# Performance work log

Measured on AMD Instinct MI355X. Metric: run time of the kernel, lower is better.

Reference implementation:

```python
import jax, jax.numpy as jnp
import numpy as np

EPS = 1e-5
HEADS, DK, DV = 8, 32, 32


def conv3x3(x, w, b):
    # regular (non-depthwise, despite the name) 3x3 conv, stride 1, padding 1
    y = jax.lax.conv_general_dilated(
        x, w, window_strides=(1, 1), padding='SAME',
        dimension_numbers=('NCHW', 'OIHW', 'NCHW'))
    return y + b[None, :, None, None]


def setup_inputs() -> dict:
    key = jax.random.key(0)
    ks = jax.random.split(key, 16)
    C = 256
    d = {}
    d['x'] = jax.random.normal(ks[0], (8, C, 32, 32), jnp.float32)
    s_lin = 1.0 / np.sqrt(C)
    s_conv = 1.0 / np.sqrt(C * 9)
    d['Wq'] = jax.random.normal(ks[1], (C, HEADS * DK), jnp.float32) * s_lin
    d['bq'] = jnp.zeros((HEADS * DK,), jnp.float32)
    d['conv_k_w'] = jax.random.normal(ks[2], (C, C, 3, 3), jnp.float32) * s_conv
    d['conv_k_b'] = jnp.zeros((C,), jnp.float32)
    d['Wk'] = jax.random.normal(ks[3], (C, HEADS * DK), jnp.float32) * s_lin
    d['bk'] = jnp.zeros((HEADS * DK,), jnp.float32)
    d['conv_v_w'] = jax.random.normal(ks[4], (C, C, 3, 3), jnp.float32) * s_conv
    d['conv_v_b'] = jnp.zeros((C,), jnp.float32)
    d['Wv'] = jax.random.normal(ks[5], (C, HEADS * DV), jnp.float32) * s_lin
    d['bv'] = jnp.zeros((HEADS * DV,), jnp.float32)
    d['Wo'] = jax.random.normal(ks[6], (HEADS * DV, C), jnp.float32) * s_lin
    d['bo'] = jnp.zeros((C,), jnp.float32)
    d['B'] = jax.random.normal(ks[7], (1, HEADS, 1024, 1024), jnp.float32) * 0.02
    return d


def reference(x, Wq, bq, conv_k_w, conv_k_b, Wk, bk, conv_v_w, conv_v_b, Wv, bv, Wo, bo, B):
    b, c, h, w = x.shape
    hw = h * w
    xr = x.reshape(b, c, hw).transpose(0, 2, 1)  # [b, hw, c]
    # F.layer_norm with normalized_shape == full shape: whole-tensor stats, no affine
    m = jnp.mean(xr)
    v = jnp.mean((xr - m) ** 2)
    xn = (xr - m) * jax.lax.rsqrt(v + EPS)

    q = (xn @ Wq + bq).reshape(b, hw, HEADS, DK).transpose(0, 2, 1, 3)  # [b,H,hw,dk]

    k = conv3x3(x, conv_k_w, conv_k_b)  # stride 1 -> same spatial size (per source)
    k = k.reshape(b, c, hw).transpose(0, 2, 1)
    k = (k @ Wk + bk).reshape(b, hw, HEADS, DK).transpose(0, 2, 1, 3)

    vv = conv3x3(x, conv_v_w, conv_v_b)
    vv = vv.reshape(b, c, hw).transpose(0, 2, 1)
    vv = (vv @ Wv + bv).reshape(b, hw, HEADS, DV).transpose(0, 2, 1, 3)

    scale = DK ** (-0.5)
    attn = jnp.einsum('bhid,bhjd->bhij', q, k) * scale + B  # [b,H,hw,hw]
    attn = jax.nn.softmax(attn, axis=-1)
    out = jnp.einsum('bhij,bhjd->bhid', attn, vv)  # [b,H,hw,dv]
    out = out.transpose(0, 2, 1, 3).reshape(b, hw, HEADS * DV)
    out = out @ Wo + bo  # [b, hw, c]
    # faithful to torch .view(b, c, h, w): raw reshape, NO transpose
    out = out.reshape(b, c, h, w)
    return out + x
```

## Files before the change

### kernel.cpp

```cpp
#include <hip/hip_runtime.h>
#include <hip/hip_bf16.h>
#include <math.h>

#define B_     8
#define C_     256
#define HW_    1024
#define NTOT   (B_*C_*HW_)
#define HEADS_ 8
#define DK_    32
#define SCALE_ 0.17677669529663687f

#define F_STATS 0
#define F_PART  16
#define F_YK2   8192
#define F_YV2   (F_YK2 + NTOT)
#define F_XB    (F_YV2 + NTOT)
#define F_WT    (F_XB + NTOT/2)
#define F_QB    (F_WT + 589824)
#define F_KB    (F_QB + NTOT/2)
#define F_VT    (F_KB + NTOT/2)

typedef float f32x4 __attribute__((ext_vector_type(4)));
typedef short short8 __attribute__((ext_vector_type(8)));

__device__ __forceinline__ short bf16s(float f) {
    __hip_bfloat16 h = __float2bfloat16(f);
    return *(short*)&h;
}
__device__ __forceinline__ unsigned pack_bf16(float a, float b) {
    unsigned ua = (unsigned short)bf16s(a);
    unsigned ub = (unsigned short)bf16s(b);
    return ua | (ub << 16);
}
__device__ __forceinline__ void gload_lds16(const short* g, short* l) {
    __builtin_amdgcn_global_load_lds(
        (const __attribute__((address_space(1))) unsigned*)g,
        (__attribute__((address_space(3))) unsigned*)l, 16, 0, 0);
}

__global__ void k_prep_x(const float* __restrict__ x, short* __restrict__ xb,
                         float* __restrict__ part) {
    __shared__ short t[32 * 258];
    __shared__ float ls[4], ls2[4];
    int b = blockIdx.x >> 5, p0 = (blockIdx.x & 31) << 5;
    int tid = threadIdx.x;
    float s = 0.f, s2 = 0.f;
    for (int i = tid; i < 256 * 32; i += 256) {
        int ci = i >> 5, p = i & 31;
        float v = x[(b * C_ + ci) * HW_ + p0 + p];
        s += v; s2 += v * v;
        t[p * 258 + ci] = bf16s(v);
    }
    for (int o = 32; o; o >>= 1) { s += __shfl_down(s, o); s2 += __shfl_down(s2, o); }
    int wid = tid >> 6, lane = tid & 63;
    if (lane == 0) { ls[wid] = s; ls2[wid] = s2; }
    __syncthreads();
    if (tid == 0) {
        float a = 0.f, bb = 0.f;
        for (int i = 0; i < 4; i++) { a += ls[i]; bb += ls2[i]; }
        part[blockIdx.x * 2] = a; part[blockIdx.x * 2 + 1] = bb;
    }
    for (int i = tid; i < 32 * 256; i += 256) {
        int p = i >> 8, ci = i & 255;
        xb[(b * HW_ + p0 + p) * C_ + ci] = t[p * 258 + ci];
    }
}

__global__ void k_stats(const float* __restrict__ part, float* __restrict__ stats) {
    __shared__ float ls[256], ls2[256];
    float s = part[2 * threadIdx.x], s2 = part[2 * threadIdx.x + 1];
    ls[threadIdx.x] = s; ls2[threadIdx.x] = s2;
    __syncthreads();
    for (int off = 128; off; off >>= 1) {
        if (threadIdx.x < off) { ls[threadIdx.x] += ls[threadIdx.x + off]; ls2[threadIdx.x] += ls2[threadIdx.x + off]; }
        __syncthreads();
    }
    if (threadIdx.x == 0) {
        float m = ls[0] / (float)NTOT;
        float var = ls2[0] / (float)NTOT - m * m;
        stats[0] = m;
        stats[1] = rsqrtf(var + 1e-5f);
    }
}

__global__ void k_prep_w(const float* __restrict__ wk, const float* __restrict__ wv,
                         short* __restrict__ wt) {
    int idx = blockIdx.x * 256 + threadIdx.x;
    int ci0 = (idx << 2) & 255;
    int rest = idx >> 6;
    int n = rest & 511, tap = rest >> 9;
    const float* src = (n < 256) ? (wk + (n * C_) * 9) : (wv + ((n - 256) * C_) * 9);
    short4 o;
    short* op = (short*)&o;
    for (int u = 0; u < 4; u++)
        op[u] = bf16s(src[(ci0 + u) * 9 + tap]);
    *(short4*)&wt[((tap * 512 + n) * C_) + ci0] = o;
}

__global__ void k_prep_pw(const float* __restrict__ Wq, const float* __restrict__ Wk,
                          const float* __restrict__ Wv, const float* __restrict__ Wo,
                          short* __restrict__ wt4) {
    __shared__ short t[64 * 66];
    int mi = blockIdx.x >> 4, tl = blockIdx.x & 15;
    int c0 = (tl >> 2) * 64, e0 = (tl & 3) * 64;
    const float* W = mi == 0 ? Wq : mi == 1 ? Wk : mi == 2 ? Wv : Wo;
    int tid = threadIdx.x;
    for (int i = tid; i < 4096; i += 256) {
        int cl = i >> 6, el = i & 63;
        t[cl * 66 + el] = bf16s(W[(c0 + cl) * 256 + e0 + el]);
    }
    __syncthreads();
    for (int i = tid; i < 4096; i += 256) {
        int el = i >> 6, cl = i & 63;
        wt4[mi * 65536 + (e0 + el) * 256 + c0 + cl] = t[cl * 66 + el];
    }
}

__global__ void k_prep_beta(const float* __restrict__ Wq, const float* __restrict__ bq,
                            const float* __restrict__ stats, float* __restrict__ beta0) {
    __shared__ float ps[1024];
    int t = threadIdx.x, e = t & 255, part = t >> 8;
    float s = 0.f;
    for (int c = part * 64; c < part * 64 + 64; c++) s += Wq[c * 256 + e];
    ps[t] = s;
    __syncthreads();
    if (t < 256) {
        float cs = ps[t] + ps[t + 256] + ps[t + 512] + ps[t + 768];
        beta0[t] = (bq[t] - stats[0] * stats[1] * cs) * SCALE_;
    }
}

__device__ __forceinline__ int a_off(int slot, int chunk) {
    int c = chunk ^ (slot & 3);
    int s = slot ^ ((slot >> 2) & 1);
    return s * 64 + c * 16;
}

__global__ __launch_bounds__(512, 4)
void k_conv_mfma(const short* __restrict__ xb, const short* __restrict__ wt,
                 const float* __restrict__ bk, const float* __restrict__ bv,
                 short* __restrict__ yk2b, short* __restrict__ yv2b) {
    __shared__ short a_sh[204 * 32];
    __shared__ short b_sh[9 * 2048];
    int bid = blockIdx.x;
    int nt = bid & 7, pt = (bid >> 3) & 7, b = bid >> 6;
    int R0 = pt * 4;
    int tid = threadIdx.x;
    int w = tid >> 6, l = tid & 63;
    int wm = w >> 1, wn = w & 1;
    int col16 = l & 15, kq = l >> 4;

    int offs[2], loffs[2];
    #pragma unroll
    for (int it = 0; it < 2; it++) {
        int i = tid + it * 512;
        if (i < 816) {
            int slot = i >> 2, chunk = i & 3;
            int ty = slot / 34, tx = slot - ty * 34;
            int Y = R0 - 1 + ty, X = tx - 1;
            offs[it] = ((unsigned)Y < 32u && (unsigned)X < 32u)
                       ? ((b * HW_ + Y * 32 + X) * C_ + chunk * 8) : -1;
            loffs[it] = a_off(slot, chunk);
        } else { offs[it] = -1; loffs[it] = -1; }
    }

    int bgoff[5];
    int nbj = 0;
    #pragma unroll 1
    for (int j = w; j < 36; j += 8) {
        int S = j * 64 + l;
        int tap = S >> 8, s = S & 255;
        int colb = s >> 2, kqs = s & 3;
        int kq2 = kqs ^ ((colb >> 1) & 3);
        bgoff[nbj++] = (tap * 512 + nt * 64 + colb) * C_ + kq2 * 8;
    }

    f32x4 acc[2][2];
    #pragma unroll
    for (int m = 0; m < 2; m++)
        #pragma unroll
        for (int n = 0; n < 2; n++) acc[m][n] = (f32x4)0.f;

    int sr[2];
    #pragma unroll
    for (int nf = 0; nf < 2; nf++) {
        int colb = wn * 32 + nf * 16 + col16;
        sr[nf] = (colb << 2) | (kq ^ ((colb >> 1) & 3));
    }

    {
        short8 sv[2];
        #pragma unroll
        for (int it = 0; it < 2; it++)
            sv[it] = (offs[it] >= 0) ? *(const short8*)(xb + offs[it]) : (short8)0;
        int jj = 0;
        #pragma unroll 1
        for (int j = w; j < 36; j += 8, jj++)
            gload_lds16(wt + bgoff[jj], b_sh + j * 512);
        #pragma unroll
        for (int it = 0; it < 2; it++)
            if (loffs[it] >= 0) *(short8*)((char*)a_sh + loffs[it]) = sv[it];
    }
    __syncthreads();

    #pragma unroll 1
    for (int step = 0; step < 8; step++) {
        const char* ab = (const char*)a_sh;
        const char* bbp = (const char*)b_sh;
        #pragma unroll
        for (int tap = 0; tap < 9; tap++) {
            const int dyi = tap / 3, dxi = tap % 3;
            short8 af[2], bf[2];
            #pragma unroll
            for (int mf = 0; mf < 2; mf++) {
                int slot = (wm + dyi) * 34 + mf * 16 + col16 + dxi;
                af[mf] = *(const short8*)(ab + a_off(slot, kq));
            }
            #pragma unroll
            for (int nf = 0; nf < 2; nf++)
                bf[nf] = *(const short8*)(bbp + tap * 4096 + sr[nf] * 16);
            #pragma unroll
            for (int mf = 0; mf < 2; mf++)
                #pragma unroll
                for (int nf = 0; nf < 2; nf++)
                    acc[mf][nf] = __builtin_amdgcn_mfma_f32_16x16x32_bf16(af[mf], bf[nf], acc[mf][nf], 0, 0, 0);
        }
        if (step < 7) {
            int ci0n = step * 32 + 32;
            __syncthreads();
            short8 sv[2];
            #pragma unroll
            for (int it = 0; it < 2; it++)
                sv[it] = (offs[it] >= 0) ? *(const short8*)(xb + offs[it] + ci0n) : (short8)0;
            int jj = 0;
            #pragma unroll 1
            for (int j = w; j < 36; j += 8, jj++)
                gload_lds16(wt + bgoff[jj] + ci0n, b_sh + j * 512);
            #pragma unroll
            for (int it = 0; it < 2; it++)
                if (loffs[it] >= 0) *(short8*)((char*)a_sh + loffs[it]) = sv[it];
            __syncthreads();
        }
    }

    const bool isv = (nt >= 4);
    short* dst = isv ? yv2b : yk2b;
    const float* bias = isv ? bv : bk;
    int cbase = (nt & 3) * 64 + wn * 32 + col16;
    #pragma unroll
    for (int nf = 0; nf < 2; nf++) {
        int co = cbase + nf * 16;
        float bi = bias[co];
        #pragma unroll
        for (int mf = 0; mf < 2; mf++) {
            #pragma unroll
            for (int r = 0; r < 4; r++) {
                int pixel = pt * 128 + wm * 32 + mf * 16 + kq * 4 + r;
                dst[(b * HW_ + pixel) * C_ + co] = bf16s(acc[mf][nf][r] + bi);
            }
        }
    }
}

__global__ void k_proj_mfma(const short* __restrict__ xb,
                            const short* __restrict__ yk2b, const short* __restrict__ yv2b,
                            const short* __restrict__ wt4,
                            const float* __restrict__ bkp, const float* __restrict__ bvp,
                            const float* __restrict__ stats, const float* __restrict__ beta0,
                            short* __restrict__ qb, short* __restrict__ kb,
                            short* __restrict__ vt) {
    __shared__ char smem[17408];
    int pj = blockIdx.x, pt = blockIdx.y, b = blockIdx.z;
    int p0 = pt * 32;
    int tid = threadIdx.x, w = tid >> 6, l = tid & 63;
    int c16 = l & 15, kq = l >> 4;

    const short* src = pj == 0 ? xb : (pj == 1 ? yk2b : yv2b);
    #pragma unroll
    for (int it = 0; it < 4; it++) {
        int i = it * 256 + tid;
        int slab = i >> 7, rem = i & 127, slot = rem >> 2, chunk = rem & 3;
        short8 v = *(const short8*)(src + ((b * HW_ + p0 + slot) * C_ + slab * 32 + chunk * 8));
        *(short8*)(smem + slab * 2048 + a_off(slot, chunk)) = v;
    }
    __syncthreads();

    const short* wt_p = wt4 + pj * 65536;
    f32x4 acc[2][4];
    #pragma unroll
    for (int m = 0; m < 2; m++)
        #pragma unroll
        for (int n = 0; n < 4; n++) acc[m][n] = (f32x4)0.f;

    for (int s = 0; s < 8; s++) {
        short8 af[2], bf[4];
        #pragma unroll
        for (int mf = 0; mf < 2; mf++)
            af[mf] = *(const short8*)(smem + s * 2048 + a_off(mf * 16 + c16, kq));
        #pragma unroll
        for (int nf = 0; nf < 4; nf++)
            bf[nf] = *(const short8*)(wt_p + (w * 64 + nf * 16 + c16) * 256 + s * 32 + kq * 8);
        #pragma unroll
        for (int mf = 0; mf < 2; mf++)
            #pragma unroll
            for (int nf = 0; nf < 4; nf++)
                acc[mf][nf] = __builtin_amdgcn_mfma_f32_16x16x32_bf16(af[mf], bf[nf], acc[mf][nf], 0, 0, 0);
    }

    float alpha = (pj == 0) ? stats[1] * SCALE_ : 1.f;
    float beta[4];
    #pragma unroll
    for (int nf = 0; nf < 4; nf++) {
        int e = w * 64 + nf * 16 + c16;
        beta[nf] = (pj == 0) ? beta0[e] : (pj == 1 ? bkp[e] : bvp[e]);
    }
    __syncthreads();

    short* rp = (short*)smem + w * 2176;
    if (pj < 2) {
        #pragma unroll
        for (int mf = 0; mf < 2; mf++)
            #pragma unroll
            for (int nf = 0; nf < 4; nf++)
                #pragma unroll
                for (int rg = 0; rg < 4; rg++) {
                    int px = mf * 16 + kq * 4 + rg, el = nf * 16 + c16;
                    rp[px * 66 + el] = bf16s(alpha * acc[mf][nf][rg] + beta[nf]);
                }
        __syncthreads();
        short* dst = (pj == 0) ? qb : kb;
        #pragma unroll
        for (int j = 0; j < 4; j++) {
            int px = j * 8 + (l >> 3), el = (l & 7) * 8;
            short8 v = *(const short8*)(rp + px * 66 + el);
            int e = w * 64 + el, h = e >> 5, d = e & 31;
            *(short8*)(dst + ((b * 8 + h) * HW_ + p0 + px) * DK_ + d) = v;
        }
    } else {
        #pragma unroll
        for (int mf = 0; mf < 2; mf++)
            #pragma unroll
            for (int nf = 0; nf < 4; nf++)
                #pragma unroll
                for (int rg = 0; rg < 4; rg++) {
                    int px = mf * 16 + kq * 4 + rg, el = nf * 16 + c16;
                    rp[el * 34 + px] = bf16s(acc[mf][nf][rg] + beta[nf]);
                }
        __syncthreads();
        #pragma unroll
        for (int j = 0; j < 4; j++) {
            int el = j * 16 + (l >> 2), px = (l & 3) * 8;
            short8 v = *(const short8*)(rp + el * 34 + px);
            int e = w * 64 + el, h = e >> 5, d = e & 31;
            *(short8*)(vt + ((b * 8 + h) * DK_ + d) * HW_ + p0 + px) = v;
        }
    }
}

__global__ __launch_bounds__(256, 4)
void k_attn(const short* __restrict__ qb, const short* __restrict__ kb,
            const short* __restrict__ vt, const float* __restrict__ Bb,
            short* __restrict__ ao) {
    __shared__ __align__(16) short Ks[128 * 32];
    __shared__ __align__(16) short Vs[32 * 128];
    int bid = blockIdx.x;
    int h = bid & 7, b = (bid >> 3) & 7, qt = bid >> 6;
    int bh = b * HEADS_ + h;
    int tid = threadIdx.x, w = tid >> 6, l = tid & 63;
    int g = l >> 4, c16 = l & 15;

    int qrow = qt * 64 + w * 16 + c16;
    short8 qf = *(const short8*)(qb + (bh * HW_ + qrow) * DK_ + g * 8);
    const float* Brow = Bb + (h * HW_ + qrow) * HW_;

    float4 breg[8];
    #pragma unroll
    for (int mt = 0; mt < 8; mt++)
        breg[mt] = *(const float4*)(Brow + mt * 16 + g * 4);

    float m_run = -1e30f, l_run = 0.f;
    f32x4 ot[2];
    ot[0] = (f32x4)0.f; ot[1] = (f32x4)0.f;

    int vrow = tid >> 4, vch = tid & 15;
    int vrow2 = (tid + 256) >> 4, vch2 = (tid + 256) & 15;
    const short* kbase = kb + bh * HW_ * DK_;

    for (int kv0 = 0; kv0 < HW_; kv0 += 128) {
        __syncthreads();
        gload_lds16(kbase + kv0 * DK_ + (w * 2) * 512 + l * 8, Ks + (w * 2) * 512);
        gload_lds16(kbase + kv0 * DK_ + (w * 2 + 1) * 512 + l * 8, Ks + (w * 2 + 1) * 512);
        {
            short8 v0 = *(const short8*)(vt + (bh * DK_ + vrow) * HW_ + kv0 + vch * 8);
            short8 v1 = *(const short8*)(vt + (bh * DK_ + vrow2) * HW_ + kv0 + vch2 * 8);
            *(short8*)((char*)Vs + vrow * 256 + ((vch * 16) ^ ((vrow & 7) << 4))) = v0;
            *(short8*)((char*)Vs + vrow2 * 256 + ((vch2 * 16) ^ ((vrow2 & 7) << 4))) = v1;
        }
        __syncthreads();

        f32x4 st[8];
        __builtin_amdgcn_s_setprio(1);
        #pragma unroll
        for (int mt = 0; mt < 8; mt++) {
            f32x4 acc;
            acc[0] = breg[mt].x; acc[1] = breg[mt].y; acc[2] = breg[mt].z; acc[3] = breg[mt].w;
            short8 kf = *(const short8*)(Ks + (mt * 16 + c16) * DK_ + g * 8);
            st[mt] = __builtin_amdgcn_mfma_f32_16x16x32_bf16(kf, qf, acc, 0, 0, 0);
        }
        __builtin_amdgcn_s_setprio(0);
        if (kv0 + 128 < HW_) {
            #pragma unroll
            for (int mt = 0; mt < 8; mt++)
                breg[mt] = *(const float4*)(Brow + kv0 + 128 + mt * 16 + g * 4);
        }

        float pmax = st[0][0];
        #pragma unroll
        for (int mt = 0; mt < 8; mt++)
            #pragma unroll
            for (int rg = 0; rg < 4; rg++) pmax = fmaxf(pmax, st[mt][rg]);
        pmax = fmaxf(pmax, __shfl_xor(pmax, 16));
        pmax = fmaxf(pmax, __shfl_xor(pmax, 32));
        if (!__all(pmax <= m_run + 8.f)) {
            float mnew = fmaxf(m_run, pmax);
            float f = __expf(m_run - mnew);
            m_run = mnew;
            l_run *= f;
            int fv = __float_as_int(f);
            #pragma unroll
            for (int rg = 0; rg < 4; rg++) {
                float fr = __int_as_float(__builtin_amdgcn_ds_bpermute((g * 4 + rg) << 2, fv));
                ot[0][rg] *= fr;
                ot[1][rg] *= fr;
            }
        }
        float s = 0.f;
        #pragma unroll
        for (int mt = 0; mt < 8; mt++)
            #pragma unroll
            for (int rg = 0; rg < 4; rg++) {
                float e_ = __expf(st[mt][rg] - m_run);
                st[mt][rg] = e_;
                s += e_;
            }
        s += __shfl_xor(s, 16);
        s += __shfl_xor(s, 32);
        l_run += s;

        short8 pa[4];
        #pragma unroll
        for (int kt = 0; kt < 4; kt++) {
            unsigned u0 = pack_bf16(st[2 * kt][0], st[2 * kt][1]);
            unsigned u1 = pack_bf16(st[2 * kt][2], st[2 * kt][3]);
            unsigned u2 = pack_bf16(st[2 * kt + 1][0], st[2 * kt + 1][1]);
            unsigned u3 = pack_bf16(st[2 * kt + 1][2], st[2 * kt + 1][3]);
            unsigned* pu = (unsigned*)&pa[kt];
            pu[0] = u0; pu[1] = u1; pu[2] = u2; pu[3] = u3;
        }

        __builtin_amdgcn_s_setprio(1);
        #pragma unroll
        for (int kt = 0; kt < 4; kt++) {
            #pragma unroll
            for (int nt = 0; nt < 2; nt++) {
                int dv = c16 + 16 * nt;
                int X0 = kt * 64 + 8 * g;
                int X1 = X0 + 32;
                int a0 = dv * 256 + ((((X0 >> 4) ^ (dv & 7)) << 4) | (X0 & 15));
                int a1 = dv * 256 + ((((X1 >> 4) ^ (dv & 7)) << 4) | (X1 & 15));
                unsigned long long lo = *(const unsigned long long*)((char*)Vs + a0);
                unsigned long long hi = *(const unsigned long long*)((char*)Vs + a1);
                short8 vf;
                *(unsigned long long*)&vf = lo;
                *((unsigned long long*)&vf + 1) = hi;
                ot[nt] = __builtin_amdgcn_mfma_f32_16x16x32_bf16(pa[kt], vf, ot[nt], 0, 0, 0);
            }
        }
        __builtin_amdgcn_s_setprio(0);
    }

    float linv = 1.f / l_run;
    int lrv = __float_as_int(linv);
    #pragma unroll
    for (int rg = 0; rg < 4; rg++) {
        float li = __int_as_float(__builtin_amdgcn_ds_bpermute((g * 4 + rg) << 2, lrv));
        int qg = qt * 64 + w * 16 + g * 4 + rg;
        #pragma unroll
        for (int nt = 0; nt < 2; nt++)
            ao[(b * HW_ + qg) * C_ + h * DK_ + nt * 16 + c16] = bf16s(ot[nt][rg] * li);
    }
}

__global__ void k_out_mfma(const short* __restrict__ aob, const short* __restrict__ wot,
                           const float* __restrict__ bo, const float* __restrict__ x,
                           float* __restrict__ out) {
    __shared__ char smem[16384];
    int pt = blockIdx.x, b = blockIdx.y;
    int p0 = pt * 32;
    int tid = threadIdx.x, w = tid >> 6, l = tid & 63;
    int c16 = l & 15, kq = l >> 4;

    #pragma unroll
    for (int it = 0; it < 4; it++) {
        int i = it * 256 + tid;
        int slab = i >> 7, rem = i & 127, slot = rem >> 2, chunk = rem & 3;
        short8 v = *(const short8*)(aob + ((b * HW_ + p0 + slot) * C_ + slab * 32 + chunk * 8));
        *(short8*)(smem + slab * 2048 + a_off(slot, chunk)) = v;
    }
    __syncthreads();

    f32x4 acc[2][4];
    #pragma unroll
    for (int m = 0; m < 2; m++)
        #pragma unroll
        for (int n = 0; n < 4; n++) acc[m][n] = (f32x4)0.f;

    for (int s = 0; s < 8; s++) {
        short8 af[2], bf[4];
        #pragma unroll
        for (int mf = 0; mf < 2; mf++)
            af[mf] = *(const short8*)(smem + s * 2048 + a_off(mf * 16 + c16, kq));
        #pragma unroll
        for (int nf = 0; nf < 4; nf++)
            bf[nf] = *(const short8*)(wot + (w * 64 + nf * 16 + c16) * 256 + s * 32 + kq * 8);
        #pragma unroll
        for (int mf = 0; mf < 2; mf++)
            #pragma unroll
            for (int nf = 0; nf < 4; nf++)
                acc[mf][nf] = __builtin_amdgcn_mfma_f32_16x16x32_bf16(af[mf], bf[nf], acc[mf][nf], 0, 0, 0);
    }

    #pragma unroll
    for (int nf = 0; nf < 4; nf++) {
        int e = w * 64 + nf * 16 + c16;
        float bov = bo[e];
        #pragma unroll
        for (int mf = 0; mf < 2; mf++) {
            #pragma unroll
            for (int rg = 0; rg < 4; rg++) {
                int px = mf * 16 + kq * 4 + rg;
                int idx = b * (C_ * HW_) + (p0 + px) * 256 + e;
                out[idx] = acc[mf][nf][rg] + bov + x[idx];
            }
        }
    }
}

extern "C" void kernel_launch(void* const* d_in, const int* in_sizes, int n_in,
                              void* d_out, int out_size, void* d_ws, size_t ws_size,
                              hipStream_t stream) {
    const float* x   = (const float*)d_in[0];
    const float* Wq  = (const float*)d_in[1];
    const float* bq  = (const float*)d_in[2];
    const float* ckw = (const float*)d_in[3];
    const float* ckb = (const float*)d_in[4];
    const float* Wk  = (const float*)d_in[5];
    const float* bk  = (const float*)d_in[6];
    const float* cvw = (const float*)d_in[7];
    const float* cvb = (const float*)d_in[8];
    const float* Wv  = (const float*)d_in[9];
    const float* bv  = (const float*)d_in[10];
    const float* Wo  = (const float*)d_in[11];
    const float* bo  = (const float*)d_in[12];
    const float* Bb  = (const float*)d_in[13];
    float* ws  = (float*)d_ws;
    float* out = (float*)d_out;

    short* xb      = (short*)(ws + F_XB);
    short* wt      = (short*)(ws + F_WT);
    short* wt4     = (short*)(ws + F_WT);
    float* beta0   = ws + F_WT + 131072;
    short* qb      = (short*)(ws + F_QB);
    short* kb      = (short*)(ws + F_KB);
    short* vt      = (short*)(ws + F_VT);
    short* yk2b    = (short*)(ws + F_YK2);
    short* yv2b    = (short*)(ws + F_YV2);
    short* aob     = (short*)(ws + F_YK2);
    short* wot     = wt4 + 3 * 65536;

    k_prep_x   <<<256,  256, 0, stream>>>(x, xb, ws + F_PART);
    k_stats    <<<1,    256, 0, stream>>>(ws + F_PART, ws + F_STATS);
    k_prep_w   <<<1152, 256, 0, stream>>>(ckw, cvw, wt);
    k_conv_mfma<<<512,  512, 0, stream>>>(xb, wt, ckb, cvb, yk2b, yv2b);
    k_prep_pw  <<<64,   256, 0, stream>>>(Wq, Wk, Wv, Wo, wt4);
    k_prep_beta<<<1,   1024, 0, stream>>>(Wq, bq, ws + F_STATS, beta0);
    k_proj_mfma<<<dim3(3, 32, 8), 256, 0, stream>>>(xb, yk2b, yv2b,
                                                    wt4, bk, bv, ws + F_STATS, beta0,
                                                    qb, kb, vt);
    k_attn     <<<1024, 256, 0, stream>>>(qb, kb, vt, Bb, aob);
    k_out_mfma <<<dim3(32, 8), 256, 0, stream>>>(aob, wot, bo, x, out);
}
```

Before: 131.5 us.

## Merge prep kernels, read K directly from global, prefetch V, use exp2

The three preparation kernels (x transpose and partial stats, conv weight reorder, pointwise weight transpose) become one launch, and the stats and beta kernels are merged, cutting launch count and serialisation. wt4 and beta0 move to their own workspace region so the conv weights are no longer overwritten. In attention, K fragments are loaded straight from global memory instead of staged through LDS, and V tiles are register-prefetched one iteration ahead. Softmax exponentials switch to exp2 with a fused log2e scale. Direct global K loads may raise latency in the QK MFMA loop.

Result: slower. 135.3 us (+2.8%).

```diff
diff --git a/kernel.cpp b/kernel.cpp
--- a/kernel.cpp
+++ b/kernel.cpp
@@ -9,6 +9,7 @@
 #define HEADS_ 8
 #define DK_    32
 #define SCALE_ 0.17677669529663687f
+#define L2E_   1.4426950408889634f
 
 #define F_STATS 0
 #define F_PART  16
@@ -19,6 +20,8 @@
 #define F_QB    (F_WT + 589824)
 #define F_KB    (F_QB + NTOT/2)
 #define F_VT    (F_KB + NTOT/2)
+#define F_WT4   (F_VT + NTOT/2)
+#define F_BETA0 (F_WT4 + 131072)
 
 typedef float f32x4 __attribute__((ext_vector_type(4)));
 typedef short short8 __attribute__((ext_vector_type(8)));
@@ -38,95 +41,92 @@
         (__attribute__((address_space(3))) unsigned*)l, 16, 0, 0);
 }
 
-__global__ void k_prep_x(const float* __restrict__ x, short* __restrict__ xb,
-                         float* __restrict__ part) {
+__global__ void k_prep_all(const float* __restrict__ x,
+                           const float* __restrict__ wk, const float* __restrict__ wv,
+                           const float* __restrict__ Wq, const float* __restrict__ Wk,
+                           const float* __restrict__ Wv, const float* __restrict__ Wo,
+                           short* __restrict__ xb, float* __restrict__ part,
+                           short* __restrict__ wt, short* __restrict__ wt4) {
     __shared__ short t[32 * 258];
     __shared__ float ls[4], ls2[4];
-    int b = blockIdx.x >> 5, p0 = (blockIdx.x & 31) << 5;
+    int bid = blockIdx.x;
     int tid = threadIdx.x;
-    float s = 0.f, s2 = 0.f;
-    for (int i = tid; i < 256 * 32; i += 256) {
-        int ci = i >> 5, p = i & 31;
-        float v = x[(b * C_ + ci) * HW_ + p0 + p];
-        s += v; s2 += v * v;
-        t[p * 258 + ci] = bf16s(v);
-    }
-    for (int o = 32; o; o >>= 1) { s += __shfl_down(s, o); s2 += __shfl_down(s2, o); }
-    int wid = tid >> 6, lane = tid & 63;
-    if (lane == 0) { ls[wid] = s; ls2[wid] = s2; }
-    __syncthreads();
-    if (tid == 0) {
-        float a = 0.f, bb = 0.f;
-        for (int i = 0; i < 4; i++) { a += ls[i]; bb += ls2[i]; }
-        part[blockIdx.x * 2] = a; part[blockIdx.x * 2 + 1] = bb;
-    }
-    for (int i = tid; i < 32 * 256; i += 256) {
-        int p = i >> 8, ci = i & 255;
-        xb[(b * HW_ + p0 + p) * C_ + ci] = t[p * 258 + ci];
-    }
-}
-
-__global__ void k_stats(const float* __restrict__ part, float* __restrict__ stats) {
-    __shared__ float ls[256], ls2[256];
-    float s = part[2 * threadIdx.x], s2 = part[2 * threadIdx.x + 1];
-    ls[threadIdx.x] = s; ls2[threadIdx.x] = s2;
+    if (bid < 256) {
+        int b = bid >> 5, p0 = (bid & 31) << 5;
+        float s = 0.f, s2 = 0.f;
+        for (int i = tid; i < 256 * 32; i += 256) {
+            int ci = i >> 5, p = i & 31;
+            float v = x[(b * C_ + ci) * HW_ + p0 + p];
+            s += v; s2 += v * v;
+            t[p * 258 + ci] = bf16s(v);
+        }
+        for (int o = 32; o; o >>= 1) { s += __shfl_down(s, o); s2 += __shfl_down(s2, o); }
+        int wid = tid >> 6, lane = tid & 63;
+        if (lane == 0) { ls[wid] = s; ls2[wid] = s2; }
+        __syncthreads();
+        if (tid == 0) {
+            float a = 0.f, bb = 0.f;
+            for (int i = 0; i < 4; i++) { a += ls[i]; bb += ls2[i]; }
+            part[bid * 2] = a; part[bid * 2 + 1] = bb;
+        }
+        for (int i = tid; i < 32 * 256; i += 256) {
+            int p = i >> 8, ci = i & 255;
+            xb[(b * HW_ + p0 + p) * C_ + ci] = t[p * 258 + ci];
+        }
+    } else if (bid < 1408) {
+        int idx = (bid - 256) * 256 + tid;
+        int ci0 = (idx << 2) & 255;
+        int rest = idx >> 6;
+        int n = rest & 511, tap = rest >> 9;
+        const float* src = (n < 256) ? (wk + (n * C_) * 9) : (wv + ((n - 256) * C_) * 9);
+        short4 o;
+        short* op = (short*)&o;
+        for (int u = 0; u < 4; u++)
+            op[u] = bf16s(src[(ci0 + u) * 9 + tap]);
+        *(short4*)&wt[((tap * 512 + n) * C_) + ci0] = o;
+    } else {
+        int b2 = bid - 1408;
+        int mi = b2 >> 4, tl = b2 & 15;
+        int c0 = (tl >> 2) * 64, e0 = (tl & 3) * 64;
+        const float* W = mi == 0 ? Wq : mi == 1 ? Wk : mi == 2 ? Wv : Wo;
+        for (int i = tid; i < 4096; i += 256) {
+            int cl = i >> 6, el = i & 63;
+            t[cl * 66 + el] = bf16s(W[(c0 + cl) * 256 + e0 + el]);
+        }
+        __syncthreads();
+        for (int i = tid; i < 4096; i += 256) {
+            int el = i >> 6, cl = i & 63;
+            wt4[mi * 65536 + (e0 + el) * 256 + c0 + cl] = t[cl * 66 + el];
+        }
+    }
+}
+
+__global__ void k_stats_beta(const float* __restrict__ part,
+                             const float* __restrict__ Wq, const float* __restrict__ bq,
+                             float* __restrict__ stats, float* __restrict__ beta0) {
+    __shared__ float ls[256], ls2[256], ps[1024], st2[2];
+    int tid = threadIdx.x;
+    if (tid < 256) { ls[tid] = part[2 * tid]; ls2[tid] = part[2 * tid + 1]; }
     __syncthreads();
     for (int off = 128; off; off >>= 1) {
-        if (threadIdx.x < off) { ls[threadIdx.x] += ls[threadIdx.x + off]; ls2[threadIdx.x] += ls2[threadIdx.x + off]; }
-        __syncthreads();
-    }
-    if (threadIdx.x == 0) {
+        if (tid < off) { ls[tid] += ls[tid + off]; ls2[tid] += ls2[tid + off]; }
+        __syncthreads();
+    }
+    if (tid == 0) {
         float m = ls[0] / (float)NTOT;
         float var = ls2[0] / (float)NTOT - m * m;
-        stats[0] = m;
-        stats[1] = rsqrtf(var + 1e-5f);
-    }
-}
-
-__global__ void k_prep_w(const float* __restrict__ wk, const float* __restrict__ wv,
-                         short* __restrict__ wt) {
-    int idx = blockIdx.x * 256 + threadIdx.x;
-    int ci0 = (idx << 2) & 255;
-    int rest = idx >> 6;
-    int n = rest & 511, tap = rest >> 9;
-    const float* src = (n < 256) ? (wk + (n * C_) * 9) : (wv + ((n - 256) * C_) * 9);
-    short4 o;
-    short* op = (short*)&o;
-    for (int u = 0; u < 4; u++)
-        op[u] = bf16s(src[(ci0 + u) * 9 + tap]);
-    *(short4*)&wt[((tap * 512 + n) * C_) + ci0] = o;
-}
-
-__global__ void k_prep_pw(const float* __restrict__ Wq, const float* __restrict__ Wk,
-                          const float* __restrict__ Wv, const float* __restrict__ Wo,
-                          short* __restrict__ wt4) {
-    __shared__ short t[64 * 66];
-    int mi = blockIdx.x >> 4, tl = blockIdx.x & 15;
-    int c0 = (tl >> 2) * 64, e0 = (tl & 3) * 64;
-    const float* W = mi == 0 ? Wq : mi == 1 ? Wk : mi == 2 ? Wv : Wo;
-    int tid = threadIdx.x;
-    for (int i = tid; i < 4096; i += 256) {
-        int cl = i >> 6, el = i & 63;
-        t[cl * 66 + el] = bf16s(W[(c0 + cl) * 256 + e0 + el]);
-    }
+        float r = rsqrtf(var + 1e-5f);
+        stats[0] = m; stats[1] = r;
+        st2[0] = m; st2[1] = r;
+    }
+    int e = tid & 255, pp = tid >> 8;
+    float s = 0.f;
+    for (int c = pp * 64; c < pp * 64 + 64; c++) s += Wq[c * 256 + e];
+    ps[tid] = s;
     __syncthreads();
-    for (int i = tid; i < 4096; i += 256) {
-        int el = i >> 6, cl = i & 63;
-        wt4[mi * 65536 + (e0 + el) * 256 + c0 + cl] = t[cl * 66 + el];
-    }
-}
-
-__global__ void k_prep_beta(const float* __restrict__ Wq, const float* __restrict__ bq,
-                            const float* __restrict__ stats, float* __restrict__ beta0) {
-    __shared__ float ps[1024];
-    int t = threadIdx.x, e = t & 255, part = t >> 8;
-    float s = 0.f;
-    for (int c = part * 64; c < part * 64 + 64; c++) s += Wq[c * 256 + e];
-    ps[t] = s;
-    __syncthreads();
-    if (t < 256) {
-        float cs = ps[t] + ps[t + 256] + ps[t + 512] + ps[t + 768];
-        beta0[t] = (bq[t] - stats[0] * stats[1] * cs) * SCALE_;
+    if (tid < 256) {
+        float cs = ps[tid] + ps[tid + 256] + ps[tid + 512] + ps[tid + 768];
+        beta0[tid] = (bq[tid] - st2[0] * st2[1] * cs) * SCALE_;
     }
 }
 
@@ -361,7 +361,6 @@
 void k_attn(const short* __restrict__ qb, const short* __restrict__ kb,
             const short* __restrict__ vt, const float* __restrict__ Bb,
             short* __restrict__ ao) {
-    __shared__ __align__(16) short Ks[128 * 32];
     __shared__ __align__(16) short Vs[32 * 128];
     int bid = blockIdx.x;
     int h = bid & 7, b = (bid >> 3) & 7, qt = bid >> 6;
@@ -386,25 +385,17 @@
     int vrow2 = (tid + 256) >> 4, vch2 = (tid + 256) & 15;
     const short* kbase = kb + bh * HW_ * DK_;
 
+    short8 v0 = *(const short8*)(vt + (bh * DK_ + vrow) * HW_ + vch * 8);
+    short8 v1 = *(const short8*)(vt + (bh * DK_ + vrow2) * HW_ + vch2 * 8);
+
     for (int kv0 = 0; kv0 < HW_; kv0 += 128) {
-        __syncthreads();
-        gload_lds16(kbase + kv0 * DK_ + (w * 2) * 512 + l * 8, Ks + (w * 2) * 512);
-        gload_lds16(kbase + kv0 * DK_ + (w * 2 + 1) * 512 + l * 8, Ks + (w * 2 + 1) * 512);
-        {
-            short8 v0 = *(const short8*)(vt + (bh * DK_ + vrow) * HW_ + kv0 + vch * 8);
-            short8 v1 = *(const short8*)(vt + (bh * DK_ + vrow2) * HW_ + kv0 + vch2 * 8);
-            *(short8*)((char*)Vs + vrow * 256 + ((vch * 16) ^ ((vrow & 7) << 4))) = v0;
-            *(short8*)((char*)Vs + vrow2 * 256 + ((vch2 * 16) ^ ((vrow2 & 7) << 4))) = v1;
-        }
-        __syncthreads();
-
         f32x4 st[8];
         __builtin_amdgcn_s_setprio(1);
         #pragma unroll
         for (int mt = 0; mt < 8; mt++) {
+            short8 kf = *(const short8*)(kbase + (kv0 + mt * 16 + c16) * DK_ + g * 8);
             f32x4 acc;
             acc[0] = breg[mt].x; acc[1] = breg[mt].y; acc[2] = breg[mt].z; acc[3] = breg[mt].w;
-            short8 kf = *(const short8*)(Ks + (mt * 16 + c16) * DK_ + g * 8);
             st[mt] = __builtin_amdgcn_mfma_f32_16x16x32_bf16(kf, qf, acc, 0, 0, 0);
         }
         __builtin_amdgcn_s_setprio(0);
@@ -423,7 +414,7 @@
         pmax = fmaxf(pmax, __shfl_xor(pmax, 32));
         if (!__all(pmax <= m_run + 8.f)) {
             float mnew = fmaxf(m_run, pmax);
-            float f = __expf(m_run - mnew);
+            float f = exp2f((m_run - mnew) * L2E_);
             m_run = mnew;
             l_run *= f;
             int fv = __float_as_int(f);
@@ -434,18 +425,29 @@
                 ot[1][rg] *= fr;
             }
         }
+        float negml = -m_run * L2E_;
         float s = 0.f;
         #pragma unroll
         for (int mt = 0; mt < 8; mt++)
             #pragma unroll
             for (int rg = 0; rg < 4; rg++) {
-                float e_ = __expf(st[mt][rg] - m_run);
+                float e_ = exp2f(fmaf(st[mt][rg], L2E_, negml));
                 st[mt][rg] = e_;
                 s += e_;
             }
         s += __shfl_xor(s, 16);
         s += __shfl_xor(s, 32);
         l_run += s;
+
+        __syncthreads();
+        *(short8*)((char*)Vs + vrow * 256 + ((vch * 16) ^ ((vrow & 7) << 4))) = v0;
+        *(short8*)((char*)Vs + vrow2 * 256 + ((vch2 * 16) ^ ((vrow2 & 7) << 4))) = v1;
+        __syncthreads();
+        if (kv0 + 128 < HW_) {
+            int nk = kv0 + 128;
+            v0 = *(const short8*)(vt + (bh * DK_ + vrow) * HW_ + nk + vch * 8);
+            v1 = *(const short8*)(vt + (bh * DK_ + vrow2) * HW_ + nk + vch2 * 8);
+        }
 
         short8 pa[4];
         #pragma unroll
@@ -568,8 +570,8 @@
 
     short* xb      = (short*)(ws + F_XB);
     short* wt      = (short*)(ws + F_WT);
-    short* wt4     = (short*)(ws + F_WT);
-    float* beta0   = ws + F_WT + 131072;
+    short* wt4     = (short*)(ws + F_WT4);
+    float* beta0   = ws + F_BETA0;
     short* qb      = (short*)(ws + F_QB);
     short* kb      = (short*)(ws + F_KB);
     short* vt      = (short*)(ws + F_VT);
@@ -578,15 +580,13 @@
     short* aob     = (short*)(ws + F_YK2);
     short* wot     = wt4 + 3 * 65536;
 
-    k_prep_x   <<<256,  256, 0, stream>>>(x, xb, ws + F_PART);
-    k_stats    <<<1,    256, 0, stream>>>(ws + F_PART, ws + F_STATS);
-    k_prep_w   <<<1152, 256, 0, stream>>>(ckw, cvw, wt);
-    k_conv_mfma<<<512,  512, 0, stream>>>(xb, wt, ckb, cvb, yk2b, yv2b);
-    k_prep_pw  <<<64,   256, 0, stream>>>(Wq, Wk, Wv, Wo, wt4);
-    k_prep_beta<<<1,   1024, 0, stream>>>(Wq, bq, ws + F_STATS, beta0);
-    k_proj_mfma<<<dim3(3, 32, 8), 256, 0, stream>>>(xb, yk2b, yv2b,
-                                                    wt4, bk, bv, ws + F_STATS, beta0,
-                                                    qb, kb, vt);
-    k_attn     <<<1024, 256, 0, stream>>>(qb, kb, vt, Bb, aob);
-    k_out_mfma <<<dim3(32, 8), 256, 0, stream>>>(aob, wot, bo, x, out);
-}
+    k_prep_all  <<<1472, 256, 0, stream>>>(x, ckw, cvw, Wq, Wk, Wv, Wo,
+                                           xb, ws + F_PART, wt, wt4);
+    k_stats_beta<<<1,   1024, 0, stream>>>(ws + F_PART, Wq, bq, ws + F_STATS, beta0);
+    k_conv_mfma <<<512,  512, 0, stream>>>(xb, wt, ckb, cvb, yk2b, yv2b);
+    k_proj_mfma <<<dim3(3, 32, 8), 256, 0, stream>>>(xb, yk2b, yv2b,
+                                                     wt4, bk, bv, ws + F_STATS, beta0,
+                                                     qb, kb, vt);
+    k_attn      <<<1024, 256, 0, stream>>>(qb, kb, vt, Bb, aob);
+    k_out_mfma  <<<dim3(32, 8), 256, 0, stream>>>(aob, wot, bo, x, out);
+}
```
